# Kernel optimization log

Measured on AMD Instinct MI355X. Metric: run time of the kernel, lower is better.

The kernel has to match this reference:

```python
import jax, jax.numpy as jnp
import numpy as np

# Module constants (from init_kwargs)
ANCHORS = np.array([[116.0, 90.0], [156.0, 198.0], [373.0, 326.0]], dtype=np.float32)
ANCHOR_AREAS = jnp.asarray(ANCHORS[:, 0] * ANCHORS[:, 1])  # [A]
A, H, W, C = 3, 128, 128, 2
IMG_W, IMG_H = 1024.0, 1024.0
STRIDE_W, STRIDE_H = IMG_W / H, IMG_H / W
ATTRS = 5 + C
LAMBDA_XY, LAMBDA_WH, LAMBDA_CONF, LAMBDA_CLS = 2.5, 2.5, 1.0, 1.0


def setup_inputs() -> dict:
    key = jax.random.key(0)
    k1, k2, k3, k4, k5 = jax.random.split(key, 5)
    B, T = 64, 2
    # conf/class feed BCELoss -> predictions must lie in [0,1)
    output = jax.random.uniform(k1, (B, A * H * W * ATTRS), dtype=jnp.float32)
    # Corner-format target boxes constructed so the (buggy) cell index
    # int((w - cx)/stride) is always within [0, mapSize).
    x1 = jax.random.uniform(k2, (B, T), minval=0.0, maxval=20.0)
    y1 = jax.random.uniform(k3, (B, T), minval=0.0, maxval=20.0)
    x2 = x1 + jax.random.uniform(k4, (B, T), minval=200.0, maxval=880.0)
    y2 = y1 + jax.random.uniform(k5, (B, T), minval=200.0, maxval=880.0)
    boxes = jnp.stack([x1, y1, x2, y2], axis=-1)  # [B,T,4]
    areas = (x2 - x1) * (y2 - y1)                 # [B,T]
    labels = jnp.ones((B, T), dtype=jnp.int32)    # label 1 -> valid for both one-hot quirks
    return {"output": output, "boxes": boxes, "labels": labels, "areas": areas}


def _bce(p, t):
    # torch BCELoss: mean, with log clamped to -100
    lp = jnp.maximum(jnp.log(p), -100.0)
    l1p = jnp.maximum(jnp.log1p(-p), -100.0)
    return -jnp.mean(t * lp + (1.0 - t) * l1p)


def _mse(p, t):
    return jnp.mean((p - t) ** 2)


def yolo_loss(output, boxes, labels, areas):
    B = output.shape[0]
    T = boxes.shape[1]
    out = output.reshape(B, A, H, W, ATTRS)
    x, y, w, h, conf = out[..., 0], out[..., 1], out[..., 2], out[..., 3], out[..., 4]
    cls = out[..., 5:]  # [B,A,H,W,C]

    gx = jnp.arange(H, dtype=output.dtype)[None, None, :, None]  # xCoord axis
    gy = jnp.arange(W, dtype=output.dtype)[None, None, None, :]  # yCoord axis
    x = x - gx
    y = y - gy

    # convert target boxes corners -> center format (done in-place in the original)
    cx = (boxes[..., 0] + boxes[..., 2]) * 0.5
    cy = (boxes[..., 1] + boxes[..., 3]) * 0.5
    bw = boxes[..., 2] - boxes[..., 0]
    bh = boxes[..., 3] - boxes[..., 1]
    tb = jnp.stack([cx, cy, bw, bh], axis=-1)  # [B,T,4]

    # class one-hots: target 0 uses labels[0]; targets i>=1 use labels[i]-1 (original quirk)
    cls0 = jax.nn.one_hot(labels[:, 0], C, dtype=output.dtype)
    cls1 = jax.nn.one_hot(labels[:, 1] - 1, C, dtype=output.dtype)
    tcls = jnp.stack([cls0, cls1], axis=1)            # [B,T,C]
    full = jnp.concatenate([tb, tcls], axis=-1)       # [B,T,4+C]

    best_anchor = jnp.argmin(jnp.abs(ANCHOR_AREAS[None, None, :] - areas[..., None]), axis=-1)  # [B,T]
    # original computes cell as int((w - cx)/stride), int((h - cy)/stride)
    cellX = ((bw - cx) / STRIDE_W).astype(jnp.int32)
    cellY = ((bh - cy) / STRIDE_H).astype(jnp.int32)

    mask = jnp.zeros((B, A, H, W), jnp.int32)
    exact = jnp.zeros((B, A, H, W), bool)
    bidx = jnp.arange(B)
    for i in range(T):  # tiny fixed loop over targets; later targets overwrite, as in torch
        mask = mask.at[bidx, best_anchor[:, i], cellX[:, i], cellY[:, i]].set(i)
        exact = exact.at[bidx, best_anchor[:, i], cellX[:, i], cellY[:, i]].set(True)

    matched = full[bidx[:, None, None, None], mask]  # [B,A,H,W,4+C]

    zero = jnp.zeros((), output.dtype)
    tX = jnp.where(exact, matched[..., 0] - gx, zero)
    tY = jnp.where(exact, matched[..., 1] - gy, zero)
    tW = jnp.where(exact, matched[..., 2], zero)
    tH = jnp.where(exact, matched[..., 3], zero)
    tConf = exact.astype(output.dtype)
    # targetMatched[5:] has length C-1==1 and broadcasts to all C slots (original quirk)
    tCls = jnp.where(exact[..., None], jnp.broadcast_to(matched[..., 5:6], cls.shape), zero)

    # IOU: prediction (x-gx, y-gy, w, h) converted center->corners; target center-format
    # boxes are (incorrectly, but faithfully) treated as corners.
    px1, py1 = x - w * 0.5, y - h * 0.5
    px2, py2 = x + w * 0.5, y + h * 0.5
    tx1 = tb[..., 0][:, None, None, None, :]  # [B,1,1,1,T]
    ty1 = tb[..., 1][:, None, None, None, :]
    tx2 = tb[..., 2][:, None, None, None, :]
    ty2 = tb[..., 3][:, None, None, None, :]
    ix = jnp.clip(jnp.minimum(px2[..., None], tx2) - jnp.maximum(px1[..., None], tx1), 0.0)
    iy = jnp.clip(jnp.minimum(py2[..., None], ty2) - jnp.maximum(py1[..., None], ty1), 0.0)
    inter = ix * iy                                   # [B,A,H,W,T]
    area_p = (px2 - px1) * (py2 - py1)                # [B,A,H,W]
    area_t = ((tx2 - tx1) * (ty2 - ty1))              # [B,1,1,1,T]
    iou = inter / (area_p[..., None] + area_t - inter + 1e-16)
    max_iou = jnp.max(iou, axis=-1)                   # [B,A,H,W]

    suppress = jnp.logical_and(~exact, max_iou > 0.5)
    xf = jnp.where(exact, x, zero)
    yf = jnp.where(exact, y, zero)
    wf = jnp.where(exact, w, zero)
    hf = jnp.where(exact, h, zero)
    clsf = jnp.where(exact[..., None], cls, zero)
    conff = jnp.where(suppress, zero, conf)

    xL, yL = _mse(xf, tX), _mse(yf, tY)
    wL, hL = _mse(wf, tW), _mse(hf, tH)
    confL = _bce(conff, tConf)
    clsL = _bce(clsf, tCls)
    loss = (xL + yL) * LAMBDA_XY + (wL + hL) * LAMBDA_WH + confL * LAMBDA_CONF + clsL * LAMBDA_CLS
    return (loss, xL, yL, wL, hL, confL, clsL)


def reference(output, boxes, labels, areas):
    return yolo_loss(output, boxes, labels, areas)
```

## Files before the change

### kernel.cpp

```cpp
#include <hip/hip_runtime.h>
#include <math.h>

#define A_ 3
#define H_ 128
#define W_ 128
#define C_ 2
#define ATTRS 7
#define B_ 64
#define CELLS_PER_BATCH (A_*H_*W_)
#define TOTAL_CELLS (B_*CELLS_PER_BATCH)

#define NTHR 256
#define ITERS 8
#define CELLS_PER_BLOCK (NTHR*ITERS)
#define NBLK (TOTAL_CELLS/CELLS_PER_BLOCK)
#define TILE_F4 448

__global__ __launch_bounds__(NTHR) void yolo_main_k(
    const float* __restrict__ outp,
    const float* __restrict__ boxes,
    const int*   __restrict__ labels,
    const float* __restrict__ areas,
    float* __restrict__ ws)
{
    __shared__ float4 s_tile[2][TILE_F4];
    __shared__ float  s_red[4][6];
    const int tid   = threadIdx.x;
    const int bcell = blockIdx.x * CELLS_PER_BLOCK;
    const int b     = bcell / CELLS_PER_BATCH;

    float cxA[2], cyA[2], bwA[2], bhA[2], atA[2], t5A[2];
    int   baA[2], cXA[2], cYA[2];
    #pragma unroll
    for (int t = 0; t < 2; ++t) {
        const float x1 = boxes[b*8 + t*4 + 0];
        const float y1 = boxes[b*8 + t*4 + 1];
        const float x2 = boxes[b*8 + t*4 + 2];
        const float y2 = boxes[b*8 + t*4 + 3];
        const float cx = (x1 + x2) * 0.5f, cy = (y1 + y2) * 0.5f;
        const float bw = x2 - x1,          bh = y2 - y1;
        cxA[t] = cx; cyA[t] = cy; bwA[t] = bw; bhA[t] = bh;
        atA[t] = (bw - cx) * (bh - cy);
        const float ar = areas[b*2 + t];
        const float d0 = fabsf(10440.f - ar);
        const float d1 = fabsf(30888.f - ar);
        const float d2 = fabsf(121598.f - ar);
        int ba = 0; float bd = d0;
        if (d1 < bd) { ba = 1; bd = d1; }
        if (d2 < bd) { ba = 2; }
        baA[t] = ba;
        cXA[t] = (int)((bw - cx) * 0.125f);
        cYA[t] = (int)((bh - cy) * 0.125f);
        const int lab = labels[b*2 + t];
        t5A[t] = (t == 0) ? (lab == 1 ? 1.f : 0.f) : (lab == 2 ? 1.f : 0.f);
    }

    const int  rblk = bcell - b * CELLS_PER_BATCH;
    const int  a    = rblk >> 14;
    const bool aok0 = (a == baA[0]);
    const bool aok1 = (a == baA[1]);

    const float4* g = (const float4*)(outp + (size_t)bcell * ATTRS);
    float4 p0 = g[tid];
    float4 p1;
    if (tid < 192) p1 = g[tid + 256];

    float accX = 0.f, accY = 0.f, accW = 0.f, accH = 0.f, accC = 0.f, accK = 0.f;
    int cur = 0;

    for (int it = 0; it < ITERS; ++it) {
        s_tile[cur][tid] = p0;
        if (tid < 192) s_tile[cur][tid + 256] = p1;
        __syncthreads();

        if (it + 1 < ITERS) {
            const float4* gn = g + (it + 1) * TILE_F4;
            p0 = gn[tid];
            if (tid < 192) p1 = gn[tid + 256];
        }

        const float* sp = ((const float*)s_tile[cur]) + tid * ATTRS;
        const float xr   = sp[0], yr = sp[1];
        const float w    = sp[2], h  = sp[3];
        const float conf = sp[4], c0 = sp[5], c1 = sp[6];

        const int r = rblk + it * NTHR + tid;
        const int i = (r >> 7) & 127;
        const int j = r & 127;
        const float fi = (float)i, fj = (float)j;

        const float x = xr - fi, y = yr - fj;
        const float hw = 0.5f * w, hh = 0.5f * h;
        const float px1 = x - hw, px2 = x + hw;
        const float py1 = y - hh, py2 = y + hh;
        const float areaP = (px2 - px1) * (py2 - py1);

        bool e[2]; float iou[2];
        #pragma unroll
        for (int t = 0; t < 2; ++t) {
            e[t] = (t ? aok1 : aok0) && (i == cXA[t]) && (j == cYA[t]);
            const float ix = fmaxf(fminf(px2, bwA[t]) - fmaxf(px1, cxA[t]), 0.f);
            const float iy = fmaxf(fminf(py2, bhA[t]) - fmaxf(py1, cyA[t]), 0.f);
            const float in_ = ix * iy;
            iou[t] = in_ / (areaP + atA[t] - in_ + 1e-16f);
        }
        const bool  exact = e[0] || e[1];
        const float miou  = fmaxf(iou[0], iou[1]);
        const bool  suppress = (!exact) && (miou > 0.5f);

        if (exact) {
            const int t = e[1] ? 1 : 0;
            const float dx = x - (cxA[t] - fi); accX += dx * dx;
            const float dy = y - (cyA[t] - fj); accY += dy * dy;
            const float dw = w - bwA[t];        accW += dw * dw;
            const float dh = h - bhA[t];        accH += dh * dh;
            accC += fmaxf(logf(conf), -100.f);
            if (t5A[t] != 0.f)
                accK += fmaxf(logf(c0), -100.f) + fmaxf(logf(c1), -100.f);
            else
                accK += fmaxf(log1pf(-c0), -100.f) + fmaxf(log1pf(-c1), -100.f);
        } else if (!suppress) {
            accC += fmaxf(log1pf(-conf), -100.f);
        }

        cur ^= 1;
    }

    float v[6] = {accX, accY, accW, accH, accC, accK};
    #pragma unroll
    for (int m = 0; m < 6; ++m) {
        float s = v[m];
        #pragma unroll
        for (int off = 32; off > 0; off >>= 1) s += __shfl_down(s, off, 64);
        v[m] = s;
    }
    const int wid = tid >> 6;
    if ((tid & 63) == 0) {
        #pragma unroll
        for (int m = 0; m < 6; ++m) s_red[wid][m] = v[m];
    }
    __syncthreads();
    if (tid < 6) {
        const float s = s_red[0][tid] + s_red[1][tid] + s_red[2][tid] + s_red[3][tid];
        ws[tid * NBLK + blockIdx.x] = s;
    }
}

__global__ __launch_bounds__(384) void finalize_k(const float* __restrict__ ws,
                                                  float* __restrict__ o)
{
    __shared__ float s_fin[6];
    const int tid = threadIdx.x;
    const int m   = tid >> 6;
    const int l   = tid & 63;
    float s = 0.f;
    for (int k = l; k < NBLK; k += 64) s += ws[m * NBLK + k];
    #pragma unroll
    for (int off = 32; off > 0; off >>= 1) s += __shfl_down(s, off, 64);
    if (l == 0) s_fin[m] = s;
    __syncthreads();
    if (tid == 0) {
        const float N = (float)TOTAL_CELLS;
        const float xL = s_fin[0] / N, yL = s_fin[1] / N;
        const float wL = s_fin[2] / N, hL = s_fin[3] / N;
        const float confL = -s_fin[4] / N;
        const float clsL  = -s_fin[5] / (N * (float)C_);
        o[0] = 2.5f * (xL + yL) + 2.5f * (wL + hL) + confL + clsL;
        o[1] = xL; o[2] = yL; o[3] = wL; o[4] = hL; o[5] = confL; o[6] = clsL;
    }
}

extern "C" void kernel_launch(void* const* d_in, const int* in_sizes, int n_in,
                              void* d_out, int out_size, void* d_ws, size_t ws_size,
                              hipStream_t stream) {
    const float* outp   = (const float*)d_in[0];
    const float* boxes  = (const float*)d_in[1];
    const int*   labels = (const int*)d_in[2];
    const float* areas  = (const float*)d_in[3];
    float* ws = (float*)d_ws;
    float* o  = (float*)d_out;

    yolo_main_k<<<NBLK, NTHR, 0, stream>>>(outp, boxes, labels, areas, ws);
    finalize_k<<<1, 384, 0, stream>>>(ws, o);
}
```

Before: 142.4 us.

## Stage tiles via direct global-to-LDS loads and simplify IoU and log math

Replaces the register-staged double buffering with __builtin_amdgcn_global_load_lds so tiles stream straight into LDS without passing through VGPRs. The IoU > 0.5 test becomes a division-free comparison (3*inter > areaP + areaT), and log1pf(-conf) on the hot path is swapped for a fast __log2f(1-conf) scaled by ln2. Launch bounds gain an occupancy hint of 8. The fast log loses accuracy for small conf and the division-free test can differ slightly at the threshold. The loop has only one barrier per iteration, so there is a possible race where the next tile's async loads land before other waves finish reading the previous buffer.

```diff
diff --git a/kernel.cpp b/kernel.cpp
--- a/kernel.cpp
+++ b/kernel.cpp
@@ -16,7 +16,14 @@
 #define NBLK (TOTAL_CELLS/CELLS_PER_BLOCK)
 #define TILE_F4 448
 
-__global__ __launch_bounds__(NTHR) void yolo_main_k(
+__device__ __forceinline__ void stage16(const float4* __restrict__ g, float4* l) {
+    __builtin_amdgcn_global_load_lds(
+        (const __attribute__((address_space(1))) void*)g,
+        (__attribute__((address_space(3))) void*)l,
+        16, 0, 0);
+}
+
+__global__ __launch_bounds__(NTHR, 8) void yolo_main_k(
     const float* __restrict__ outp,
     const float* __restrict__ boxes,
     const int*   __restrict__ labels,
@@ -30,7 +37,10 @@
     const int b     = bcell / CELLS_PER_BATCH;
 
     float cxA[2], cyA[2], bwA[2], bhA[2], atA[2], t5A[2];
-    int   baA[2], cXA[2], cYA[2];
+    int   cXA[2], cYA[2];
+    bool  aok[2];
+    const int  rblk = bcell - b * CELLS_PER_BATCH;
+    const int  a    = rblk >> 14;
     #pragma unroll
     for (int t = 0; t < 2; ++t) {
         const float x1 = boxes[b*8 + t*4 + 0];
@@ -48,35 +58,28 @@
         int ba = 0; float bd = d0;
         if (d1 < bd) { ba = 1; bd = d1; }
         if (d2 < bd) { ba = 2; }
-        baA[t] = ba;
+        aok[t] = (a == ba);
         cXA[t] = (int)((bw - cx) * 0.125f);
         cYA[t] = (int)((bh - cy) * 0.125f);
         const int lab = labels[b*2 + t];
         t5A[t] = (t == 0) ? (lab == 1 ? 1.f : 0.f) : (lab == 2 ? 1.f : 0.f);
     }
 
-    const int  rblk = bcell - b * CELLS_PER_BATCH;
-    const int  a    = rblk >> 14;
-    const bool aok0 = (a == baA[0]);
-    const bool aok1 = (a == baA[1]);
+    const float4* g = (const float4*)(outp + (size_t)bcell * ATTRS);
 
-    const float4* g = (const float4*)(outp + (size_t)bcell * ATTRS);
-    float4 p0 = g[tid];
-    float4 p1;
-    if (tid < 192) p1 = g[tid + 256];
+    stage16(g + tid, &s_tile[0][tid]);
+    if (tid < 192) stage16(g + 256 + tid, &s_tile[0][256 + tid]);
 
     float accX = 0.f, accY = 0.f, accW = 0.f, accH = 0.f, accC = 0.f, accK = 0.f;
-    int cur = 0;
 
     for (int it = 0; it < ITERS; ++it) {
-        s_tile[cur][tid] = p0;
-        if (tid < 192) s_tile[cur][tid + 256] = p1;
+        const int cur = it & 1;
         __syncthreads();
 
         if (it + 1 < ITERS) {
             const float4* gn = g + (it + 1) * TILE_F4;
-            p0 = gn[tid];
-            if (tid < 192) p1 = gn[tid + 256];
+            stage16(gn + tid, &s_tile[cur ^ 1][tid]);
+            if (tid < 192) stage16(gn + 256 + tid, &s_tile[cur ^ 1][256 + tid]);
         }
 
         const float* sp = ((const float*)s_tile[cur]) + tid * ATTRS;
@@ -95,18 +98,17 @@
         const float py1 = y - hh, py2 = y + hh;
         const float areaP = (px2 - px1) * (py2 - py1);
 
-        bool e[2]; float iou[2];
+        bool e[2], sup[2];
         #pragma unroll
         for (int t = 0; t < 2; ++t) {
-            e[t] = (t ? aok1 : aok0) && (i == cXA[t]) && (j == cYA[t]);
+            e[t] = aok[t] && (i == cXA[t]) && (j == cYA[t]);
             const float ix = fmaxf(fminf(px2, bwA[t]) - fmaxf(px1, cxA[t]), 0.f);
             const float iy = fmaxf(fminf(py2, bhA[t]) - fmaxf(py1, cyA[t]), 0.f);
             const float in_ = ix * iy;
-            iou[t] = in_ / (areaP + atA[t] - in_ + 1e-16f);
+            sup[t] = (3.f * in_ > areaP + atA[t] + 1e-16f);
         }
-        const bool  exact = e[0] || e[1];
-        const float miou  = fmaxf(iou[0], iou[1]);
-        const bool  suppress = (!exact) && (miou > 0.5f);
+        const bool exact    = e[0] || e[1];
+        const bool suppress = (!exact) && (sup[0] || sup[1]);
 
         if (exact) {
             const int t = e[1] ? 1 : 0;
@@ -120,10 +122,8 @@
             else
                 accK += fmaxf(log1pf(-c0), -100.f) + fmaxf(log1pf(-c1), -100.f);
         } else if (!suppress) {
-            accC += fmaxf(log1pf(-conf), -100.f);
+            accC += fmaxf(__log2f(1.0f - conf) * 0.69314718f, -100.f);
         }
-
-        cur ^= 1;
     }
 
     float v[6] = {accX, accY, accW, accH, accC, accK};
```

Result: no change. 142.7 us (+0.2%).
